# Optimization experiments

Hardware: AMD Instinct MI355X
Metric: run time of the kernel (lower is better)

## Reference

```python
import jax, jax.numpy as jnp
import numpy as np

# 7-point Suzuki-Yoshida weights used by the module
_W1 = 0.78451361047756
_W2 = 0.235573213359357
_W3 = -1.17767998417887
_W4 = 1.0 - 2.0 * (_W1 + _W2 + _W3)
SY_WEIGHTS = [_W1, _W2, _W3, _W4, _W3, _W2, _W1]
NRESPA = 2

B, N, D, C = 32, 131072, 3, 5


def setup_inputs() -> dict:
    key = jax.random.key(0)
    k1, k2, k3 = jax.random.split(key, 3)
    return {
        "pos": jax.random.normal(k1, (B, N, D), dtype=jnp.float32),
        "mom": jax.random.normal(k2, (B, N, D), dtype=jnp.float32) * 0.5,
        "mas": jnp.ones((B, N), dtype=jnp.float32),
        "kbt": jnp.ones((B,), dtype=jnp.float32),
        "dtm": jnp.ones((B,), dtype=jnp.float32),
        "pos_nhc": jnp.zeros((B, C), dtype=jnp.float32),
        "mom_nhc": jax.random.normal(k3, (B, C), dtype=jnp.float32) * 0.1,
        "mas_nhc": jnp.ones((B, C), dtype=jnp.float32),
        "stp": jnp.float32(0.002),
    }


def reference(pos, mom, mas, kbt, dtm, pos_nhc, mom_nhc, mas_nhc, stp):
    n_atm, n_dim = pos.shape[1], pos.shape[2]
    nchain = mom_nhc.shape[1]
    dof = jnp.asarray(n_atm * n_dim, dtype=kbt.dtype)  # ddof = 0

    def g_fn(mom_, mom_nhc_):
        # forces on thermostat chain: g[:,0] from atomic KE, g[:,j>0] from chain KE
        kin_nhc = mom_nhc_ * mom_nhc_ / mas_nhc            # [B, C]
        g_rest = kin_nhc[:, :-1] - kbt[:, None]            # [B, C-1]
        g0 = jnp.sum(mom_ * mom_ / mas[:, :, None], axis=(1, 2)) - kbt * dof  # [B]
        return jnp.concatenate([g0[:, None], g_rest], axis=1)  # [B, C]

    def chain_pass(mom_c, g, dea):
        # sequential update down the chain (j = C-2 .. 0); C is small and fixed
        for j in range(nchain - 2, -1, -1):
            f = jnp.exp(-mom_c[:, j + 1] / mas_nhc[:, j + 1] * (dea / 4))
            mom_c = mom_c.at[:, j].set((mom_c[:, j] * f + g[:, j] * (dea / 2)) * f)
        return mom_c

    def substep(mom_, pos_nhc_, mom_nhc_, w):
        dea = dtm * (stp * w / NRESPA)  # [B]
        # First half: g computed from the pre-step chain momenta (constant over loop,
        # matching the original code which never writes mom back into the dict here).
        g = g_fn(mom_, mom_nhc_)
        mc = mom_nhc_.at[:, -1].add(g[:, -1] * (dea / 2))
        mc = chain_pass(mc, g, dea)
        # Drift of chain positions and scaling of atomic momenta
        pos_nhc_ = pos_nhc_ + mc / mas_nhc * dea[:, None]
        mom_ = mom_ * jnp.exp(-mc[:, 0] / mas_nhc[:, 0] * dea)[:, None, None]
        # Second half: g recomputed with the rescaled atomic momenta but the
        # ORIGINAL chain momenta (faithful to the source, which reads out[mom_nhc]
        # from the unmodified dict).
        g2 = g_fn(mom_, mom_nhc_)
        mc = chain_pass(mc, g2, dea)
        mc = mc.at[:, -1].add(g2[:, -1] * (dea / 2))
        return mom_, pos_nhc_, mc

    for _ in range(NRESPA):
        for w in SY_WEIGHTS:
            mom, pos_nhc, mom_nhc = substep(mom, pos_nhc, mom_nhc, w)
    return mom, pos_nhc, mom_nhc
```

## Files before the change

### kernel.cpp

```cpp
#include <hip/hip_runtime.h>

#define NCH 5

__global__ __launch_bounds__(256) void nhc_reduce(
    const float* __restrict__ mom, const float* __restrict__ mas,
    float* __restrict__ partials, int n_atoms, int groups_per_batch,
    int blocks_per_batch)
{
    const int b = blockIdx.y;
    const int t = blockIdx.x * blockDim.x + threadIdx.x;

    float s = 0.0f;
    if (t < groups_per_batch) {
        const float4* mom4 = (const float4*)(mom + (size_t)b * n_atoms * 3);
        const float4* mas4 = (const float4*)(mas + (size_t)b * n_atoms);
        float4 p0 = mom4[3 * t + 0];
        float4 p1 = mom4[3 * t + 1];
        float4 p2 = mom4[3 * t + 2];
        float4 m  = mas4[t];
        s = (p0.x * p0.x + p0.y * p0.y + p0.z * p0.z) / m.x
          + (p0.w * p0.w + p1.x * p1.x + p1.y * p1.y) / m.y
          + (p1.z * p1.z + p1.w * p1.w + p2.x * p2.x) / m.z
          + (p2.y * p2.y + p2.z * p2.z + p2.w * p2.w) / m.w;
    }

    #pragma unroll
    for (int off = 32; off > 0; off >>= 1) s += __shfl_down(s, off, 64);
    __shared__ float lds[4];
    const int lane = threadIdx.x & 63, wv = threadIdx.x >> 6;
    if (lane == 0) lds[wv] = s;
    __syncthreads();
    if (threadIdx.x == 0)
        partials[(size_t)b * blocks_per_batch + blockIdx.x] =
            lds[0] + lds[1] + lds[2] + lds[3];
}

__global__ __launch_bounds__(256) void nhc_chain_scale(
    const float* __restrict__ mom, const float* __restrict__ partials,
    const float* __restrict__ kbt, const float* __restrict__ dtm,
    const float* __restrict__ pos_nhc, const float* __restrict__ mom_nhc,
    const float* __restrict__ mas_nhc, const float* __restrict__ stp,
    float* __restrict__ out_mom, float* __restrict__ out_posnhc,
    float* __restrict__ out_momnhc,
    int bpb_red, int n4_per_batch, float dof)
{
    const int b = blockIdx.y;
    __shared__ float s_scale;

    if (threadIdx.x < 64) {
        const int lane = threadIdx.x;
        float ke = 0.0f;
        for (int i = lane; i < bpb_red; i += 64)
            ke += partials[(size_t)b * bpb_red + i];
        #pragma unroll
        for (int off = 32; off > 0; off >>= 1) ke += __shfl_down(ke, off, 64);

        if (lane == 0) {
            constexpr double W1 = 0.78451361047756;
            constexpr double W2 = 0.235573213359357;
            constexpr double W3 = -1.17767998417887;
            constexpr double W4 = 1.0 - 2.0 * (W1 + W2 + W3);
            const float syw[7] = {(float)W1, (float)W2, (float)W3, (float)W4,
                                  (float)W3, (float)W2, (float)W1};

            const float kb = kbt[b], dt = dtm[b], st = stp[0];
            float pnh[NCH], mnh[NCH], qn[NCH];
            #pragma unroll
            for (int c = 0; c < NCH; ++c) {
                pnh[c] = pos_nhc[b * NCH + c];
                mnh[c] = mom_nhc[b * NCH + c];
                qn[c]  = mas_nhc[b * NCH + c];
            }

            float Scum = 1.0f;
            for (int r = 0; r < 14; ++r) {
                const float w   = syw[r % 7];
                const float dea = dt * (st * w * 0.5f);
                const float de2 = dea * 0.5f;
                const float de4 = dea * 0.25f;

                float g[NCH], mc[NCH];
                g[0] = ke - kb * dof;
                #pragma unroll
                for (int j = 1; j < NCH; ++j)
                    g[j] = mnh[j - 1] * mnh[j - 1] / qn[j - 1] - kb;
                #pragma unroll
                for (int c = 0; c < NCH; ++c) mc[c] = mnh[c];

                mc[NCH - 1] += g[NCH - 1] * de2;
                #pragma unroll
                for (int j = NCH - 2; j >= 0; --j) {
                    const float f = expf(-mc[j + 1] / qn[j + 1] * de4);
                    mc[j] = (mc[j] * f + g[j] * de2) * f;
                }

                #pragma unroll
                for (int c = 0; c < NCH; ++c) pnh[c] += mc[c] / qn[c] * dea;
                const float s = expf(-mc[0] / qn[0] * dea);
                Scum *= s;
                ke   *= s * s;

                g[0] = ke - kb * dof;
                #pragma unroll
                for (int j = NCH - 2; j >= 0; --j) {
                    const float f = expf(-mc[j + 1] / qn[j + 1] * de4);
                    mc[j] = (mc[j] * f + g[j] * de2) * f;
                }
                mc[NCH - 1] += g[NCH - 1] * de2;

                #pragma unroll
                for (int c = 0; c < NCH; ++c) mnh[c] = mc[c];
            }

            s_scale = Scum;
            if (blockIdx.x == 0) {
                #pragma unroll
                for (int c = 0; c < NCH; ++c) {
                    out_posnhc[b * NCH + c] = pnh[c];
                    out_momnhc[b * NCH + c] = mnh[c];
                }
            }
        }
    }
    __syncthreads();

    const float s = s_scale;
    const float4* in4 = (const float4*)mom + (size_t)b * n4_per_batch;
    float4*       o4  = (float4*)out_mom   + (size_t)b * n4_per_batch;
    const int stride = gridDim.x * blockDim.x;
    for (int i = blockIdx.x * blockDim.x + threadIdx.x; i < n4_per_batch;
         i += stride) {
        float4 v = in4[i];
        v.x *= s; v.y *= s; v.z *= s; v.w *= s;
        o4[i] = v;
    }
}

extern "C" void kernel_launch(void* const* d_in, const int* in_sizes, int n_in,
                              void* d_out, int out_size, void* d_ws, size_t ws_size,
                              hipStream_t stream) {
    const float* mom     = (const float*)d_in[1];
    const float* mas     = (const float*)d_in[2];
    const float* kbt     = (const float*)d_in[3];
    const float* dtm     = (const float*)d_in[4];
    const float* pos_nhc = (const float*)d_in[5];
    const float* mom_nhc = (const float*)d_in[6];
    const float* mas_nhc = (const float*)d_in[7];
    const float* stp     = (const float*)d_in[8];

    const int B  = in_sizes[3];
    const int ND = in_sizes[1] / B;
    const int N  = in_sizes[2] / B;
    (void)n_in; (void)ws_size; (void)out_size;
    const float dof = (float)ND;

    const int groups_per_batch = N / 4;
    const int blocks_per_batch = (groups_per_batch + 255) / 256;

    float* partials = (float*)d_ws;

    float* out_f       = (float*)d_out;
    float* out_posnhc  = out_f + (size_t)B * ND;
    float* out_momnhc  = out_posnhc + (size_t)B * NCH;

    nhc_reduce<<<dim3(blocks_per_batch, B), 256, 0, stream>>>(
        mom, mas, partials, N, groups_per_batch, blocks_per_batch);

    const int n4 = ND / 4;
    nhc_chain_scale<<<dim3(64, B), 256, 0, stream>>>(
        mom, partials, kbt, dtm, pos_nhc, mom_nhc, mas_nhc, stp,
        out_f, out_posnhc, out_momnhc, blocks_per_batch, n4, dof);
}
```

Before: 176.2 us.

## Fuse reduction and scaling into one kernel with cross-block flag sync

Merges the kinetic-energy reduction and the chain/scale pass into a single launch. Each block keeps its slice of momenta in registers (12 float4 per thread) and publishes its partial sum to workspace with a value-plus-complement check word. It then spin-waits for the other 31 partials of its batch, runs the thermostat chain and writes the scaled momenta straight from registers. This removes the second read of the momentum array and one kernel launch. In exchange it relies on all 1024 blocks being resident at once, with a slow recompute fallback if the wait times out. Stale flags left in workspace from an earlier call can also be read as valid, and the block counts are hardcoded to this problem size.

```diff
diff --git a/kernel.cpp b/kernel.cpp
--- a/kernel.cpp
+++ b/kernel.cpp
@@ -2,60 +2,97 @@
 
 #define NCH 5
 
-__global__ __launch_bounds__(256) void nhc_reduce(
+__global__ __launch_bounds__(256, 4) void nhc_fused(
     const float* __restrict__ mom, const float* __restrict__ mas,
-    float* __restrict__ partials, int n_atoms, int groups_per_batch,
-    int blocks_per_batch)
-{
-    const int b = blockIdx.y;
-    const int t = blockIdx.x * blockDim.x + threadIdx.x;
-
-    float s = 0.0f;
-    if (t < groups_per_batch) {
-        const float4* mom4 = (const float4*)(mom + (size_t)b * n_atoms * 3);
-        const float4* mas4 = (const float4*)(mas + (size_t)b * n_atoms);
-        float4 p0 = mom4[3 * t + 0];
-        float4 p1 = mom4[3 * t + 1];
-        float4 p2 = mom4[3 * t + 2];
-        float4 m  = mas4[t];
-        s = (p0.x * p0.x + p0.y * p0.y + p0.z * p0.z) / m.x
-          + (p0.w * p0.w + p1.x * p1.x + p1.y * p1.y) / m.y
-          + (p1.z * p1.z + p1.w * p1.w + p2.x * p2.x) / m.z
-          + (p2.y * p2.y + p2.z * p2.z + p2.w * p2.w) / m.w;
-    }
-
-    #pragma unroll
-    for (int off = 32; off > 0; off >>= 1) s += __shfl_down(s, off, 64);
-    __shared__ float lds[4];
-    const int lane = threadIdx.x & 63, wv = threadIdx.x >> 6;
-    if (lane == 0) lds[wv] = s;
-    __syncthreads();
-    if (threadIdx.x == 0)
-        partials[(size_t)b * blocks_per_batch + blockIdx.x] =
-            lds[0] + lds[1] + lds[2] + lds[3];
-}
-
-__global__ __launch_bounds__(256) void nhc_chain_scale(
-    const float* __restrict__ mom, const float* __restrict__ partials,
     const float* __restrict__ kbt, const float* __restrict__ dtm,
     const float* __restrict__ pos_nhc, const float* __restrict__ mom_nhc,
     const float* __restrict__ mas_nhc, const float* __restrict__ stp,
     float* __restrict__ out_mom, float* __restrict__ out_posnhc,
     float* __restrict__ out_momnhc,
-    int bpb_red, int n4_per_batch, float dof)
+    unsigned int* __restrict__ sig_part, unsigned int* __restrict__ sig_chk,
+    int n4_per_batch, int nm4_per_batch, float dof)
 {
-    const int b = blockIdx.y;
+    const int bid = blockIdx.x;
+    const int b   = bid >> 5;
+    const int x   = bid & 31;
+    const int g   = x * blockDim.x + threadIdx.x;
+
+    const float4* mom4 = (const float4*)mom + (size_t)b * n4_per_batch + 12 * (size_t)g;
+    const float4* mas4 = (const float4*)mas + (size_t)b * nm4_per_batch + 4 * (size_t)g;
+
+    float4 P[12];
+    float ke = 0.0f;
+    #pragma unroll
+    for (int q = 0; q < 4; ++q) {
+        const float4 m = mas4[q];
+        const float4 a = mom4[3 * q + 0];
+        const float4 c = mom4[3 * q + 1];
+        const float4 d = mom4[3 * q + 2];
+        P[3 * q + 0] = a; P[3 * q + 1] = c; P[3 * q + 2] = d;
+        ke += (a.x * a.x + a.y * a.y + a.z * a.z) / m.x
+            + (a.w * a.w + c.x * c.x + c.y * c.y) / m.y
+            + (c.z * c.z + c.w * c.w + d.x * d.x) / m.z
+            + (d.y * d.y + d.z * d.z + d.w * d.w) / m.w;
+    }
+
+    #pragma unroll
+    for (int off = 32; off > 0; off >>= 1) ke += __shfl_down(ke, off, 64);
+    __shared__ float lds[4];
     __shared__ float s_scale;
+    const int lane = threadIdx.x & 63, wv = threadIdx.x >> 6;
+    if (lane == 0) lds[wv] = ke;
+    __syncthreads();
+    if (threadIdx.x == 0) {
+        const float pblk = lds[0] + lds[1] + lds[2] + lds[3];
+        const unsigned int pb = __float_as_uint(pblk);
+        __hip_atomic_store(&sig_part[bid], pb, __ATOMIC_RELAXED,
+                           __HIP_MEMORY_SCOPE_AGENT);
+        __hip_atomic_store(&sig_chk[bid], ~pb, __ATOMIC_RELEASE,
+                           __HIP_MEMORY_SCOPE_AGENT);
+    }
 
     if (threadIdx.x < 64) {
-        const int lane = threadIdx.x;
-        float ke = 0.0f;
-        for (int i = lane; i < bpb_red; i += 64)
-            ke += partials[(size_t)b * bpb_red + i];
+        float t = 0.0f;
+        if (threadIdx.x < 32) {
+            const int j = threadIdx.x;
+            const int i = b * 32 + j;
+            unsigned int pb = 0u;
+            bool got = false;
+            for (int it = 0; it < 4096; ++it) {
+                const unsigned int ck =
+                    __hip_atomic_load(&sig_chk[i], __ATOMIC_ACQUIRE,
+                                      __HIP_MEMORY_SCOPE_AGENT);
+                pb = __hip_atomic_load(&sig_part[i], __ATOMIC_RELAXED,
+                                       __HIP_MEMORY_SCOPE_AGENT);
+                if (ck == ~pb) { got = true; break; }
+                __builtin_amdgcn_s_sleep(2);
+            }
+            if (got) {
+                t = __uint_as_float(pb);
+            } else {
+                const float4* bm4 = (const float4*)mom +
+                    (size_t)b * n4_per_batch + (size_t)j * 3072;
+                const float4* bs4 = (const float4*)mas +
+                    (size_t)b * nm4_per_batch + (size_t)j * 1024;
+                float acc = 0.0f;
+                for (int mi = 0; mi < 1024; ++mi) {
+                    const float4 m = bs4[mi];
+                    const float4 a = bm4[3 * mi + 0];
+                    const float4 c = bm4[3 * mi + 1];
+                    const float4 d = bm4[3 * mi + 2];
+                    acc += (a.x * a.x + a.y * a.y + a.z * a.z) / m.x
+                         + (a.w * a.w + c.x * c.x + c.y * c.y) / m.y
+                         + (c.z * c.z + c.w * c.w + d.x * d.x) / m.z
+                         + (d.y * d.y + d.z * d.z + d.w * d.w) / m.w;
+                }
+                t = acc;
+            }
+        }
         #pragma unroll
-        for (int off = 32; off > 0; off >>= 1) ke += __shfl_down(ke, off, 64);
-
-        if (lane == 0) {
+        for (int off = 32; off > 0; off >>= 1) t += __shfl_down(t, off, 64);
+
+        if (threadIdx.x == 0) {
+            float kin = t;
             constexpr double W1 = 0.78451361047756;
             constexpr double W2 = 0.235573213359357;
             constexpr double W3 = -1.17767998417887;
@@ -79,41 +116,41 @@
                 const float de2 = dea * 0.5f;
                 const float de4 = dea * 0.25f;
 
-                float g[NCH], mc[NCH];
-                g[0] = ke - kb * dof;
+                float gg[NCH], mc[NCH];
+                gg[0] = kin - kb * dof;
                 #pragma unroll
                 for (int j = 1; j < NCH; ++j)
-                    g[j] = mnh[j - 1] * mnh[j - 1] / qn[j - 1] - kb;
+                    gg[j] = mnh[j - 1] * mnh[j - 1] / qn[j - 1] - kb;
                 #pragma unroll
                 for (int c = 0; c < NCH; ++c) mc[c] = mnh[c];
 
-                mc[NCH - 1] += g[NCH - 1] * de2;
+                mc[NCH - 1] += gg[NCH - 1] * de2;
                 #pragma unroll
                 for (int j = NCH - 2; j >= 0; --j) {
                     const float f = expf(-mc[j + 1] / qn[j + 1] * de4);
-                    mc[j] = (mc[j] * f + g[j] * de2) * f;
+                    mc[j] = (mc[j] * f + gg[j] * de2) * f;
                 }
 
                 #pragma unroll
                 for (int c = 0; c < NCH; ++c) pnh[c] += mc[c] / qn[c] * dea;
                 const float s = expf(-mc[0] / qn[0] * dea);
                 Scum *= s;
-                ke   *= s * s;
-
-                g[0] = ke - kb * dof;
+                kin  *= s * s;
+
+                gg[0] = kin - kb * dof;
                 #pragma unroll
                 for (int j = NCH - 2; j >= 0; --j) {
                     const float f = expf(-mc[j + 1] / qn[j + 1] * de4);
-                    mc[j] = (mc[j] * f + g[j] * de2) * f;
-                }
-                mc[NCH - 1] += g[NCH - 1] * de2;
+                    mc[j] = (mc[j] * f + gg[j] * de2) * f;
+                }
+                mc[NCH - 1] += gg[NCH - 1] * de2;
 
                 #pragma unroll
                 for (int c = 0; c < NCH; ++c) mnh[c] = mc[c];
             }
 
             s_scale = Scum;
-            if (blockIdx.x == 0) {
+            if (x == 0) {
                 #pragma unroll
                 for (int c = 0; c < NCH; ++c) {
                     out_posnhc[b * NCH + c] = pnh[c];
@@ -125,14 +162,12 @@
     __syncthreads();
 
     const float s = s_scale;
-    const float4* in4 = (const float4*)mom + (size_t)b * n4_per_batch;
-    float4*       o4  = (float4*)out_mom   + (size_t)b * n4_per_batch;
-    const int stride = gridDim.x * blockDim.x;
-    for (int i = blockIdx.x * blockDim.x + threadIdx.x; i < n4_per_batch;
-         i += stride) {
-        float4 v = in4[i];
+    float4* o4 = (float4*)out_mom + (size_t)b * n4_per_batch + 12 * (size_t)g;
+    #pragma unroll
+    for (int k = 0; k < 12; ++k) {
+        float4 v = P[k];
         v.x *= s; v.y *= s; v.z *= s; v.w *= s;
-        o4[i] = v;
+        o4[k] = v;
     }
 }
 
@@ -154,20 +189,17 @@
     (void)n_in; (void)ws_size; (void)out_size;
     const float dof = (float)ND;
 
-    const int groups_per_batch = N / 4;
-    const int blocks_per_batch = (groups_per_batch + 255) / 256;
-
-    float* partials = (float*)d_ws;
-
-    float* out_f       = (float*)d_out;
-    float* out_posnhc  = out_f + (size_t)B * ND;
-    float* out_momnhc  = out_posnhc + (size_t)B * NCH;
-
-    nhc_reduce<<<dim3(blocks_per_batch, B), 256, 0, stream>>>(
-        mom, mas, partials, N, groups_per_batch, blocks_per_batch);
-
-    const int n4 = ND / 4;
-    nhc_chain_scale<<<dim3(64, B), 256, 0, stream>>>(
-        mom, partials, kbt, dtm, pos_nhc, mom_nhc, mas_nhc, stp,
-        out_f, out_posnhc, out_momnhc, blocks_per_batch, n4, dof);
+    const int n4  = ND / 4;
+    const int nm4 = N / 4;
+
+    unsigned int* sig_part = (unsigned int*)d_ws;
+    unsigned int* sig_chk  = sig_part + 1024;
+
+    float* out_f      = (float*)d_out;
+    float* out_posnhc = out_f + (size_t)B * ND;
+    float* out_momnhc = out_posnhc + (size_t)B * NCH;
+
+    nhc_fused<<<dim3(32 * B), dim3(256), 0, stream>>>(
+        mom, mas, kbt, dtm, pos_nhc, mom_nhc, mas_nhc, stp,
+        out_f, out_posnhc, out_momnhc, sig_part, sig_chk, n4, nm4, dof);
 }
```

New measurement: 235.5 us. 33.6% more time.

## Prefetch momentum before chain solve and coarsen reduction blocks to 2048 atoms

Applied to the files above, without the earlier changes.

The scale kernel now loads its six float4 momentum values per thread into registers before the serial thermostat-chain computation, so the memory reads overlap the single-thread exp chain instead of waiting behind the barrier. The reduction kernel switches from one float4 group per thread to eight strided float3 atom loads per thread over 2048 atoms per block, cutting the number of blocks and partials. The chain also uses __expf instead of expf. In exchange, the fast path assumes the per-batch size divides exactly into the launch grid, reduction assumes N is a multiple of 2048, and float3 loads are less vectorized.

```diff
diff --git a/kernel.cpp b/kernel.cpp
--- a/kernel.cpp
+++ b/kernel.cpp
@@ -4,34 +4,30 @@
 
 __global__ __launch_bounds__(256) void nhc_reduce(
     const float* __restrict__ mom, const float* __restrict__ mas,
-    float* __restrict__ partials, int n_atoms, int groups_per_batch,
-    int blocks_per_batch)
+    float* __restrict__ partials, int n_atoms, int nd)
 {
-    const int b = blockIdx.y;
-    const int t = blockIdx.x * blockDim.x + threadIdx.x;
+    const int b    = blockIdx.y;
+    const int base = blockIdx.x * 2048;
+    const float* momb = mom + (size_t)b * nd;
+    const float* masb = mas + (size_t)b * n_atoms;
 
-    float s = 0.0f;
-    if (t < groups_per_batch) {
-        const float4* mom4 = (const float4*)(mom + (size_t)b * n_atoms * 3);
-        const float4* mas4 = (const float4*)(mas + (size_t)b * n_atoms);
-        float4 p0 = mom4[3 * t + 0];
-        float4 p1 = mom4[3 * t + 1];
-        float4 p2 = mom4[3 * t + 2];
-        float4 m  = mas4[t];
-        s = (p0.x * p0.x + p0.y * p0.y + p0.z * p0.z) / m.x
-          + (p0.w * p0.w + p1.x * p1.x + p1.y * p1.y) / m.y
-          + (p1.z * p1.z + p1.w * p1.w + p2.x * p2.x) / m.z
-          + (p2.y * p2.y + p2.z * p2.z + p2.w * p2.w) / m.w;
+    float ke = 0.0f;
+    #pragma unroll
+    for (int r = 0; r < 8; ++r) {
+        const int a = base + r * 256 + threadIdx.x;
+        const float3 p = *(const float3*)(momb + 3 * (size_t)a);
+        const float  m = masb[a];
+        ke += (p.x * p.x + p.y * p.y + p.z * p.z) / m;
     }
 
     #pragma unroll
-    for (int off = 32; off > 0; off >>= 1) s += __shfl_down(s, off, 64);
+    for (int off = 32; off > 0; off >>= 1) ke += __shfl_down(ke, off, 64);
     __shared__ float lds[4];
     const int lane = threadIdx.x & 63, wv = threadIdx.x >> 6;
-    if (lane == 0) lds[wv] = s;
+    if (lane == 0) lds[wv] = ke;
     __syncthreads();
     if (threadIdx.x == 0)
-        partials[(size_t)b * blocks_per_batch + blockIdx.x] =
+        partials[(size_t)b * gridDim.x + blockIdx.x] =
             lds[0] + lds[1] + lds[2] + lds[3];
 }
 
@@ -44,18 +40,35 @@
     float* __restrict__ out_momnhc,
     int bpb_red, int n4_per_batch, float dof)
 {
-    const int b = blockIdx.y;
+    const int b   = blockIdx.y;
+    const int tid = threadIdx.x;
+    const float4* in4 = (const float4*)mom   + (size_t)b * n4_per_batch;
+    float4*       o4  = (float4*)out_mom     + (size_t)b * n4_per_batch;
+    const int i0     = blockIdx.x * 256 + tid;
+    const int stride = gridDim.x * 256;
+
+    const bool fast = (6 * stride == n4_per_batch);
+    float4 v0, v1, v2, v3, v4, v5;
+    if (fast) {
+        v0 = in4[i0];
+        v1 = in4[i0 + 1 * stride];
+        v2 = in4[i0 + 2 * stride];
+        v3 = in4[i0 + 3 * stride];
+        v4 = in4[i0 + 4 * stride];
+        v5 = in4[i0 + 5 * stride];
+    }
+
     __shared__ float s_scale;
 
-    if (threadIdx.x < 64) {
-        const int lane = threadIdx.x;
-        float ke = 0.0f;
-        for (int i = lane; i < bpb_red; i += 64)
-            ke += partials[(size_t)b * bpb_red + i];
+    if (tid < 64) {
+        float t = 0.0f;
+        for (int i = tid; i < bpb_red; i += 64)
+            t += partials[(size_t)b * bpb_red + i];
         #pragma unroll
-        for (int off = 32; off > 0; off >>= 1) ke += __shfl_down(ke, off, 64);
+        for (int off = 32; off > 0; off >>= 1) t += __shfl_down(t, off, 64);
 
-        if (lane == 0) {
+        if (tid == 0) {
+            float kin = t;
             constexpr double W1 = 0.78451361047756;
             constexpr double W2 = 0.235573213359357;
             constexpr double W3 = -1.17767998417887;
@@ -79,34 +92,34 @@
                 const float de2 = dea * 0.5f;
                 const float de4 = dea * 0.25f;
 
-                float g[NCH], mc[NCH];
-                g[0] = ke - kb * dof;
+                float gg[NCH], mc[NCH];
+                gg[0] = kin - kb * dof;
                 #pragma unroll
                 for (int j = 1; j < NCH; ++j)
-                    g[j] = mnh[j - 1] * mnh[j - 1] / qn[j - 1] - kb;
+                    gg[j] = mnh[j - 1] * mnh[j - 1] / qn[j - 1] - kb;
                 #pragma unroll
                 for (int c = 0; c < NCH; ++c) mc[c] = mnh[c];
 
-                mc[NCH - 1] += g[NCH - 1] * de2;
+                mc[NCH - 1] += gg[NCH - 1] * de2;
                 #pragma unroll
                 for (int j = NCH - 2; j >= 0; --j) {
-                    const float f = expf(-mc[j + 1] / qn[j + 1] * de4);
-                    mc[j] = (mc[j] * f + g[j] * de2) * f;
+                    const float f = __expf(-mc[j + 1] / qn[j + 1] * de4);
+                    mc[j] = (mc[j] * f + gg[j] * de2) * f;
                 }
 
                 #pragma unroll
                 for (int c = 0; c < NCH; ++c) pnh[c] += mc[c] / qn[c] * dea;
-                const float s = expf(-mc[0] / qn[0] * dea);
+                const float s = __expf(-mc[0] / qn[0] * dea);
                 Scum *= s;
-                ke   *= s * s;
+                kin  *= s * s;
 
-                g[0] = ke - kb * dof;
+                gg[0] = kin - kb * dof;
                 #pragma unroll
                 for (int j = NCH - 2; j >= 0; --j) {
-                    const float f = expf(-mc[j + 1] / qn[j + 1] * de4);
-                    mc[j] = (mc[j] * f + g[j] * de2) * f;
+                    const float f = __expf(-mc[j + 1] / qn[j + 1] * de4);
+                    mc[j] = (mc[j] * f + gg[j] * de2) * f;
                 }
-                mc[NCH - 1] += g[NCH - 1] * de2;
+                mc[NCH - 1] += gg[NCH - 1] * de2;
 
                 #pragma unroll
                 for (int c = 0; c < NCH; ++c) mnh[c] = mc[c];
@@ -125,14 +138,19 @@
     __syncthreads();
 
     const float s = s_scale;
-    const float4* in4 = (const float4*)mom + (size_t)b * n4_per_batch;
-    float4*       o4  = (float4*)out_mom   + (size_t)b * n4_per_batch;
-    const int stride = gridDim.x * blockDim.x;
-    for (int i = blockIdx.x * blockDim.x + threadIdx.x; i < n4_per_batch;
-         i += stride) {
-        float4 v = in4[i];
-        v.x *= s; v.y *= s; v.z *= s; v.w *= s;
-        o4[i] = v;
+    if (fast) {
+        v0.x *= s; v0.y *= s; v0.z *= s; v0.w *= s; o4[i0]              = v0;
+        v1.x *= s; v1.y *= s; v1.z *= s; v1.w *= s; o4[i0 + 1 * stride] = v1;
+        v2.x *= s; v2.y *= s; v2.z *= s; v2.w *= s; o4[i0 + 2 * stride] = v2;
+        v3.x *= s; v3.y *= s; v3.z *= s; v3.w *= s; o4[i0 + 3 * stride] = v3;
+        v4.x *= s; v4.y *= s; v4.z *= s; v4.w *= s; o4[i0 + 4 * stride] = v4;
+        v5.x *= s; v5.y *= s; v5.z *= s; v5.w *= s; o4[i0 + 5 * stride] = v5;
+    } else {
+        for (int i = i0; i < n4_per_batch; i += stride) {
+            float4 v = in4[i];
+            v.x *= s; v.y *= s; v.z *= s; v.w *= s;
+            o4[i] = v;
+        }
     }
 }
 
@@ -154,17 +172,16 @@
     (void)n_in; (void)ws_size; (void)out_size;
     const float dof = (float)ND;
 
-    const int groups_per_batch = N / 4;
-    const int blocks_per_batch = (groups_per_batch + 255) / 256;
+    const int blocks_per_batch = N / 2048;
 
     float* partials = (float*)d_ws;
 
-    float* out_f       = (float*)d_out;
-    float* out_posnhc  = out_f + (size_t)B * ND;
-    float* out_momnhc  = out_posnhc + (size_t)B * NCH;
+    float* out_f      = (float*)d_out;
+    float* out_posnhc = out_f + (size_t)B * ND;
+    float* out_momnhc = out_posnhc + (size_t)B * NCH;
 
     nhc_reduce<<<dim3(blocks_per_batch, B), 256, 0, stream>>>(
-        mom, mas, partials, N, groups_per_batch, blocks_per_batch);
+        mom, mas, partials, N, ND);
 
     const int n4 = ND / 4;
     nhc_chain_scale<<<dim3(64, B), 256, 0, stream>>>(
```

New measurement: 177.3 us. No clear change (+0.6%).
